# Performance work log

Measured on AMD Instinct MI355X. Metric: run time of the kernel, lower is better.

The kernel has to match this reference:

```python
import jax, jax.numpy as jnp
import numpy as np

N = 10000        # total nodes in batch
E = 320000       # total edges (before self-loops)
D_IN = 128       # node_dim
H_DIM = 64       # hidden_dim
HEADS = 4
B = 64           # number of graphs
NUM_EDGES = 1024 # actor output dim


def _lin(k, i, o):
    return jax.random.normal(k, (i, o), jnp.float32) / np.sqrt(i)


def setup_inputs() -> dict:
    key = jax.random.key(0)
    ks = jax.random.split(key, 32)
    x = jax.random.normal(ks[0], (N, D_IN), jnp.float32)
    edge_index = jax.random.randint(ks[1], (2, E), 0, N, dtype=jnp.int64)
    batch = jnp.sort(jax.random.randint(ks[2], (N,), 0, B, dtype=jnp.int64))
    inp = dict(x=x, edge_index=edge_index, batch=batch)
    # GAT layer 1: in=D_IN, heads=4, out=H_DIM, concat
    inp['W1'] = _lin(ks[3], D_IN, HEADS * H_DIM)
    inp['as1'] = jax.random.normal(ks[4], (HEADS, H_DIM), jnp.float32) * 0.1
    inp['ad1'] = jax.random.normal(ks[5], (HEADS, H_DIM), jnp.float32) * 0.1
    inp['b1'] = jnp.zeros((HEADS * H_DIM,), jnp.float32)
    # GAT layer 2: in=4*H_DIM, heads=4, out=H_DIM, concat
    inp['W2'] = _lin(ks[6], HEADS * H_DIM, HEADS * H_DIM)
    inp['as2'] = jax.random.normal(ks[7], (HEADS, H_DIM), jnp.float32) * 0.1
    inp['ad2'] = jax.random.normal(ks[8], (HEADS, H_DIM), jnp.float32) * 0.1
    inp['b2'] = jnp.zeros((HEADS * H_DIM,), jnp.float32)
    # GAT layer 3: in=4*H_DIM, heads=1, out=H_DIM, mean (concat=False)
    inp['W3'] = _lin(ks[9], HEADS * H_DIM, H_DIM)
    inp['as3'] = jax.random.normal(ks[10], (1, H_DIM), jnp.float32) * 0.1
    inp['ad3'] = jax.random.normal(ks[11], (1, H_DIM), jnp.float32) * 0.1
    inp['b3'] = jnp.zeros((H_DIM,), jnp.float32)
    # actor MLP
    inp['Wa1'] = _lin(ks[12], H_DIM, H_DIM); inp['ba1'] = jnp.zeros((H_DIM,), jnp.float32)
    inp['Wa2'] = _lin(ks[13], H_DIM, NUM_EDGES); inp['ba2'] = jnp.zeros((NUM_EDGES,), jnp.float32)
    # critic MLP
    inp['Wc1'] = _lin(ks[14], H_DIM, H_DIM); inp['bc1'] = jnp.zeros((H_DIM,), jnp.float32)
    inp['Wc2'] = _lin(ks[15], H_DIM, 1); inp['bc2'] = jnp.zeros((1,), jnp.float32)
    return inp


def gat_layer(x, src, dst, W, a_src, a_dst, bias, heads, out_dim, concat):
    # PyG GATConv: linear -> edge attention -> per-dst softmax -> scatter-add
    n = x.shape[0]
    h = (x @ W).reshape(n, heads, out_dim)            # [N,H,D]
    s = (h * a_src).sum(-1)                           # [N,H] attention src term
    d = (h * a_dst).sum(-1)                           # [N,H]
    e = jax.nn.leaky_relu(s[src] + d[dst], 0.2)       # [Eall,H]
    m = jax.ops.segment_max(e, dst, num_segments=n)   # stable softmax per dst node
    w = jnp.exp(e - m[dst])
    alpha = w / jax.ops.segment_sum(w, dst, num_segments=n)[dst]
    agg = jax.ops.segment_sum(h[src] * alpha[..., None], dst, num_segments=n)  # [N,H,D]
    o = agg.reshape(n, heads * out_dim) if concat else agg.mean(axis=1)
    return o + bias


def forward(x, edge_index, batch, W1, as1, ad1, b1, W2, as2, ad2, b2,
            W3, as3, ad3, b3, Wa1, ba1, Wa2, ba2, Wc1, bc1, Wc2, bc2):
    n = x.shape[0]
    loop = jnp.arange(n, dtype=edge_index.dtype)
    src = jnp.concatenate([edge_index[0], loop])      # add_self_loops=True (PyG default)
    dst = jnp.concatenate([edge_index[1], loop])
    h = jax.nn.relu(gat_layer(x, src, dst, W1, as1, ad1, b1, HEADS, H_DIM, True))
    h = jax.nn.relu(gat_layer(h, src, dst, W2, as2, ad2, b2, HEADS, H_DIM, True))
    h = jax.nn.relu(gat_layer(h, src, dst, W3, as3, ad3, b3, 1, H_DIM, False))
    # global_mean_pool
    counts = jax.ops.segment_sum(jnp.ones((n,), h.dtype), batch, num_segments=B)
    pooled = jax.ops.segment_sum(h, batch, num_segments=B) / jnp.maximum(counts, 1.0)[:, None]
    # heads (dropout is identity at inference)
    action = jnp.tanh(jax.nn.relu(pooled @ Wa1 + ba1) @ Wa2 + ba2)
    value = jax.nn.relu(pooled @ Wc1 + bc1) @ Wc2 + bc2
    return action, value


def reference(x, edge_index, batch, W1, as1, ad1, b1, W2, as2, ad2, b2,
              W3, as3, ad3, b3, Wa1, ba1, Wa2, ba2, Wc1, bc1, Wc2, bc2):
    return forward(x, edge_index, batch, W1, as1, ad1, b1, W2, as2, ad2, b2,
                   W3, as3, ad3, b3, Wa1, ba1, Wa2, ba2, Wc1, bc1, Wc2, bc2)
```

## Files before the change

### kernel.cpp

```cpp
#include <hip/hip_runtime.h>
#include <hip/hip_bf16.h>

#define NN 10000
#define EE 320000
#define EALL (EE + NN)
#define BG 64
#define AOUT 1024

#define WTOT 191361
#define NX (NN * 128)
#define XV (NX / 8)
#define NSF 262144
#define NSI 131072

#define DRANGE 640
#define DNB 16
#define NSEG 64
#define ESEG 5157

typedef __hip_bfloat16 bf16;
typedef __attribute__((ext_vector_type(8))) short bf16x8;
typedef __attribute__((ext_vector_type(4))) float f32x4;

__device__ __forceinline__ unsigned short f2bf(float f) {
    bf16 h = __float2bfloat16(f);
    return *reinterpret_cast<unsigned short*>(&h);
}
__device__ __forceinline__ float bf2f(unsigned short u) {
    bf16 h;
    *reinterpret_cast<unsigned short*>(&h) = u;
    return __bfloat162float(h);
}
__device__ __forceinline__ int f_isfp32(const int* flags) {
    return (flags[2] > 0 || flags[3] > 50000) ? 1 : 0;
}

__global__ void k_detect(const unsigned short* __restrict__ x, const unsigned int* __restrict__ ei,
                         int* __restrict__ flags) {
    int i = blockIdx.x * 256 + threadIdx.x;
    bool nanp = false, zp = false, odd = false;
    if (i < NSF) {
        unsigned short h = x[i];
        nanp = (h & 0x7F80u) == 0x7F80u;
        zp = ((i & 1) == 0) && (h == 0);
    } else if (i < NSF + NSI) {
        int j = i - NSF;
        odd = ei[2 * j + 1] != 0u;
    }
    unsigned long long bn = __ballot(nanp);
    unsigned long long bz = __ballot(zp);
    unsigned long long bo = __ballot(odd);
    if ((threadIdx.x & 63) == 0) {
        if (bn) atomicAdd(&flags[2], __popcll(bn));
        if (bz) atomicAdd(&flags[3], __popcll(bz));
        if (bo) atomicOr(&flags[1], 1);
    }
}

struct WPtrs { const void* p[20]; };
__global__ void k_cvt_all(WPtrs wp, const void* __restrict__ xsrc,
                          const void* __restrict__ eisrc, const void* __restrict__ bsrc,
                          float* __restrict__ wf, int* __restrict__ ei32, int* __restrict__ b32,
                          unsigned short* __restrict__ x16,
                          unsigned short* __restrict__ w1t, unsigned short* __restrict__ w2t,
                          unsigned short* __restrict__ w3t,
                          const int* __restrict__ flags) {
    const int sz[20] = {32768,256,256,256,65536,256,256,256,16384,64,64,64,4096,64,65536,1024,4096,64,64,1};
    int i = blockIdx.x * 256 + threadIdx.x;
    const int ff = f_isfp32(flags), fi = flags[1];
    if (i < WTOT) {
        int seg = 0, off = 0;
        while (i - off >= sz[seg]) { off += sz[seg]; seg++; }
        const void* src = wp.p[seg];
        int k = i - off;
        wf[i] = ff ? ((const float*)src)[k] : __bfloat162float(((const bf16*)src)[k]);
        return;
    }
    i -= WTOT;
    if (i < EE) {
        int j = i * 2;
        if (fi) {
            int2 v = ((const int2*)eisrc)[i];
            ei32[j] = v.x; ei32[j + 1] = v.y;
        } else {
            const long long* e8 = (const long long*)eisrc;
            ei32[j] = (int)e8[j]; ei32[j + 1] = (int)e8[j + 1];
        }
        return;
    }
    i -= EE;
    if (i < NN) { b32[i] = fi ? ((const int*)bsrc)[i] : (int)((const long long*)bsrc)[i]; return; }
    i -= NN;
    if (i < XV) {
        int k = i * 8;
        if (ff) {
            const float4* xs = (const float4*)((const float*)xsrc + k);
            float4 a = xs[0], b = xs[1];
            union { unsigned short u16[8]; uint4 v; } pk;
            pk.u16[0] = f2bf(a.x); pk.u16[1] = f2bf(a.y);
            pk.u16[2] = f2bf(a.z); pk.u16[3] = f2bf(a.w);
            pk.u16[4] = f2bf(b.x); pk.u16[5] = f2bf(b.y);
            pk.u16[6] = f2bf(b.z); pk.u16[7] = f2bf(b.w);
            *(uint4*)&x16[k] = pk.v;
        } else {
            *(uint4*)&x16[k] = ((const uint4*)xsrc)[i];
        }
        return;
    }
    i -= XV;
    if (i < 32768) {
        int k = i >> 8, c = i & 255;
        float v = ff ? ((const float*)wp.p[0])[i] : __bfloat162float(((const bf16*)wp.p[0])[i]);
        w1t[c * 128 + k] = f2bf(v);
        return;
    }
    i -= 32768;
    if (i < 65536) {
        int k = i >> 8, c = i & 255;
        float v = ff ? ((const float*)wp.p[4])[i] : __bfloat162float(((const bf16*)wp.p[4])[i]);
        w2t[c * 256 + k] = f2bf(v);
        return;
    }
    i -= 65536;
    if (i < 16384) {
        int k = i >> 6, c = i & 63;
        float v = ff ? ((const float*)wp.p[8])[i] : __bfloat162float(((const bf16*)wp.p[8])[i]);
        w3t[c * 256 + k] = f2bf(v);
    }
}
#define CVT_TOT (WTOT + EE + NN + XV + 32768 + 65536 + 16384)

__global__ __launch_bounds__(256) void k_fuse1(const int* __restrict__ ei, int* __restrict__ partial,
                                               const unsigned short* __restrict__ A16,
                                               const unsigned short* __restrict__ WT16,
                                               const float* __restrict__ asf,
                                               const float* __restrict__ adf,
                                               unsigned short* __restrict__ C16,
                                               float* __restrict__ sb, float* __restrict__ db) {
    __shared__ int bins[DRANGE];
    constexpr int LDW = 40;
    __shared__ unsigned short As[64 * LDW];
    __shared__ unsigned short Bs[64 * LDW];
    const int t = threadIdx.x;
    if (blockIdx.x < DNB * NSEG) {
        const int r0 = (blockIdx.x >> 6) * DRANGE;
        const int sg = blockIdx.x & 63;
        for (int i = t; i < DRANGE; i += 256) bins[i] = 0;
        __syncthreads();
        const int e1 = min(sg * ESEG + ESEG, EALL);
        for (int e = sg * ESEG + t; e < e1; e += 256) {
            int dst = (e < EE) ? ei[EE + e] : (e - EE);
            unsigned rel = dst - r0;
            if (rel < DRANGE) atomicAdd(&bins[rel], 1);
        }
        __syncthreads();
        for (int i = t; i < DRANGE; i += 256)
            partial[blockIdx.x * DRANGE + i] = bins[i];
        return;
    }
    constexpr int K = 128, M = 256, H = M / 64;
    const int u = blockIdx.x - DNB * NSEG;
    const int bx = u % 157;
    const int hh = u / 157;
    const int row0 = bx * 64;
    const int col0 = hh * 64;
    const int wv = t >> 6;
    const int lane = t & 63;
    const int m = lane & 15;
    const int q = lane >> 4;
    const int srow = t >> 2;
    const int skoff = (t & 3) * 8;

    f32x4 acc[4] = {};
    for (int k0 = 0; k0 < K; k0 += 32) {
        {
            int grow = row0 + srow;
            uint4 av = make_uint4(0u, 0u, 0u, 0u);
            if (grow < NN) av = *(const uint4*)&A16[(size_t)grow * K + k0 + skoff];
            *(uint4*)&As[srow * LDW + skoff] = av;
            uint4 bv = *(const uint4*)&WT16[(size_t)(col0 + srow) * K + k0 + skoff];
            *(uint4*)&Bs[srow * LDW + skoff] = bv;
        }
        __syncthreads();
        bf16x8 af = *(const bf16x8*)&As[(16 * wv + m) * LDW + q * 8];
#pragma unroll
        for (int ct = 0; ct < 4; ct++) {
            bf16x8 bfv = *(const bf16x8*)&Bs[(16 * ct + m) * LDW + q * 8];
            acc[ct] = __builtin_amdgcn_mfma_f32_16x16x32_bf16(af, bfv, acc[ct], 0, 0, 0);
        }
        __syncthreads();
    }
    float asv[4], adv[4];
#pragma unroll
    for (int ct = 0; ct < 4; ct++) {
        asv[ct] = asf[hh * 64 + 16 * ct + m];
        adv[ct] = adf[hh * 64 + 16 * ct + m];
    }
#pragma unroll
    for (int reg = 0; reg < 4; reg++) {
        int row = row0 + 16 * wv + q * 4 + reg;
        float ps = 0.f, pd = 0.f;
        if (row < NN) {
#pragma unroll
            for (int ct = 0; ct < 4; ct++) {
                float v = acc[ct][reg];
                C16[(size_t)row * M + col0 + 16 * ct + m] = f2bf(v);
                ps += v * asv[ct];
                pd += v * adv[ct];
            }
        }
#pragma unroll
        for (int off = 1; off < 16; off <<= 1) {
            ps += __shfl_xor(ps, off);
            pd += __shfl_xor(pd, off);
        }
        if (m == 0 && row < NN) { sb[row * H + hh] = ps; db[row * H + hh] = pd; }
    }
}

__global__ void k_seg(const int* __restrict__ partial, int* __restrict__ deg,
                      int* __restrict__ segpre) {
    int bin = blockIdx.x * 256 + threadIdx.x;
    if (bin >= NN) return;
    int r = bin / DRANGE, rel = bin - r * DRANGE;
    int s = 0;
    for (int sg = 0; sg < NSEG; sg++) {
        int idx = (r * NSEG + sg) * DRANGE + rel;
        int v = partial[idx];
        segpre[idx] = s;
        s += v;
    }
    deg[bin] = s;
}

__global__ void k_scan4(const int* __restrict__ deg, int* __restrict__ rowstart,
                        const int* __restrict__ batch, int* __restrict__ gstart) {
    __shared__ int part[1024];
    const int t = threadIdx.x;
    if (t <= BG) {
        int lo = 0, hi = NN;
        while (lo < hi) { int mid = (lo + hi) >> 1; if (batch[mid] < t) lo = mid + 1; else hi = mid; }
        gstart[t] = lo;
    }
    const int base = t * 10;
    int local[10];
    int s = 0;
    for (int i = 0; i < 10; i++) {
        int idx = base + i;
        int v = (idx < NN) ? deg[idx] : 0;
        local[i] = s; s += v;
    }
    part[t] = s; __syncthreads();
    for (int off = 1; off < 1024; off <<= 1) {
        int v = (t >= off) ? part[t - off] : 0;
        __syncthreads();
        part[t] += v;
        __syncthreads();
    }
    int pre = (t == 0) ? 0 : part[t - 1];
    for (int i = 0; i < 10; i++) {
        int idx = base + i;
        if (idx < NN) rowstart[idx] = pre + local[i];
    }
    if (t == 1023) rowstart[NN] = part[1023];
}

__global__ __launch_bounds__(256) void k_scatter3(const int* __restrict__ ei,
                                                  const int* __restrict__ rowstart,
                                                  const int* __restrict__ segpre,
                                                  int* __restrict__ ssrc) {
    __shared__ int cur[DRANGE];
    const int r0 = blockIdx.x * DRANGE;
    const int sg = blockIdx.y;
    for (int i = threadIdx.x; i < DRANGE; i += 256) {
        int bin = r0 + i;
        cur[i] = (bin < NN) ? rowstart[bin] + segpre[(blockIdx.x * NSEG + sg) * DRANGE + i] : 0;
    }
    __syncthreads();
    const int e1 = min(sg * ESEG + ESEG, EALL);
    for (int e = sg * ESEG + threadIdx.x; e < e1; e += 256) {
        int dst = (e < EE) ? ei[EE + e] : (e - EE);
        unsigned rel = dst - r0;
        if (rel < DRANGE) {
            int src = (e < EE) ? ei[e] : dst;
            int pos = atomicAdd(&cur[rel], 1);
            ssrc[pos] = src;
        }
    }
}

template<int K, int M>
__global__ __launch_bounds__(256) void k_gemm(const unsigned short* __restrict__ A16,
                                              const unsigned short* __restrict__ WT16,
                                              const float* __restrict__ asf,
                                              const float* __restrict__ adf,
                                              unsigned short* __restrict__ C16,
                                              float* __restrict__ sb, float* __restrict__ db) {
    constexpr int BK = 32;
    constexpr int H = M / 64;
    constexpr int LDW = 40;
    __shared__ unsigned short As[64 * LDW];
    __shared__ unsigned short Bs[64 * LDW];
    const int row0 = blockIdx.x * 64;
    const int col0 = blockIdx.y * 64;
    const int hh = blockIdx.y;
    const int t = threadIdx.x;
    const int wv = t >> 6;
    const int lane = t & 63;
    const int m = lane & 15;
    const int q = lane >> 4;
    const int srow = t >> 2;
    const int skoff = (t & 3) * 8;

    f32x4 acc[4] = {};

    for (int k0 = 0; k0 < K; k0 += BK) {
        {
            int grow = row0 + srow;
            uint4 av = make_uint4(0u, 0u, 0u, 0u);
            if (grow < NN) av = *(const uint4*)&A16[(size_t)grow * K + k0 + skoff];
            *(uint4*)&As[srow * LDW + skoff] = av;
            uint4 bv = *(const uint4*)&WT16[(size_t)(col0 + srow) * K + k0 + skoff];
            *(uint4*)&Bs[srow * LDW + skoff] = bv;
        }
        __syncthreads();
        bf16x8 af = *(const bf16x8*)&As[(16 * wv + m) * LDW + q * 8];
#pragma unroll
        for (int ct = 0; ct < 4; ct++) {
            bf16x8 bfv = *(const bf16x8*)&Bs[(16 * ct + m) * LDW + q * 8];
            acc[ct] = __builtin_amdgcn_mfma_f32_16x16x32_bf16(af, bfv, acc[ct], 0, 0, 0);
        }
        __syncthreads();
    }

    float asv[4], adv[4];
#pragma unroll
    for (int ct = 0; ct < 4; ct++) {
        asv[ct] = asf[hh * 64 + 16 * ct + m];
        adv[ct] = adf[hh * 64 + 16 * ct + m];
    }
#pragma unroll
    for (int reg = 0; reg < 4; reg++) {
        int row = row0 + 16 * wv + q * 4 + reg;
        float ps = 0.f, pd = 0.f;
        if (row < NN) {
#pragma unroll
            for (int ct = 0; ct < 4; ct++) {
                float v = acc[ct][reg];
                C16[(size_t)row * M + col0 + 16 * ct + m] = f2bf(v);
                ps += v * asv[ct];
                pd += v * adv[ct];
            }
        }
#pragma unroll
        for (int off = 1; off < 16; off <<= 1) {
            ps += __shfl_xor(ps, off);
            pd += __shfl_xor(pd, off);
        }
        if (m == 0 && row < NN) { sb[row * H + hh] = ps; db[row * H + hh] = pd; }
    }
}

template<int H>
__global__ void k_agg(const unsigned short* __restrict__ hbuf16, const float* __restrict__ sb,
                      const float* __restrict__ db, const int* __restrict__ rowstart,
                      const int* __restrict__ ssrc, const float* __restrict__ bias,
                      unsigned short* __restrict__ out16) {
    constexpr int M = H * 64;
    constexpr int LH = (H == 4) ? 2 : 0;
    constexpr int CG = M / 8;
    constexpr int LCG = (H == 4) ? 5 : 3;
    const int n = blockIdx.x;
    const int tid = threadIdx.x;
    const int start = rowstart[n], end = rowstart[n + 1];
    const int slot = tid >> LH;
    const int hh = tid & (H - 1);
    const int cg = tid & (CG - 1);
    const int eg = tid >> LCG;
    const int chh = (H == 4) ? (cg >> 3) : 0;
    __shared__ float red[M];
    __shared__ float sm[H], sws[H];
    __shared__ float wl[64 * H];
    __shared__ int srcl[64];
    __shared__ float accbuf[8 * M];
    const float dn = db[n * H + hh];

    float mymax = -3e38f;
    for (int p = start + slot; p < end; p += 64) {
        float e = sb[ssrc[p] * H + hh] + dn;
        e = e > 0.f ? e : 0.2f * e;
        mymax = fmaxf(mymax, e);
    }
    red[tid] = mymax; __syncthreads();
    for (int off = M / 2; off >= H; off >>= 1) {
        if (tid < off) red[tid] = fmaxf(red[tid], red[tid + off]);
        __syncthreads();
    }
    if (tid < H) sm[tid] = red[tid];
    __syncthreads();
    const float mh = sm[hh];

    float wsum = 0.f;
    float acc[8] = {};
    for (int c = start; c < end; c += 64) {
        const int cn = min(64, end - c);
        __syncthreads();
        if (slot < cn) {
            int s = ssrc[c + slot];
            float e = sb[s * H + hh] + dn;
            e = e > 0.f ? e : 0.2f * e;
            float wv = __expf(e - mh);
            wl[slot * H + hh] = wv;
            wsum += wv;
            if (hh == 0) srcl[slot] = s;
        }
        __syncthreads();
#pragma unroll 2
        for (int j = eg; j < cn; j += 8) {
            float wv = wl[j * H + chh];
            const bf16x8 v = *(const bf16x8*)&hbuf16[(size_t)srcl[j] * M + cg * 8];
#pragma unroll
            for (int i = 0; i < 8; i++)
                acc[i] += wv * bf2f((unsigned short)v[i]);
        }
    }

    {
        float* ab = &accbuf[eg * M + cg * 8];
#pragma unroll
        for (int i = 0; i < 8; i++) ab[i] = acc[i];
    }
    red[tid] = wsum; __syncthreads();
    for (int off = M / 2; off >= H; off >>= 1) {
        if (tid < off) red[tid] += red[tid + off];
        __syncthreads();
    }
    if (tid < H) sws[tid] = red[tid];
    __syncthreads();

    float o = 0.f;
#pragma unroll
    for (int e8 = 0; e8 < 8; e8++) o += accbuf[e8 * M + tid];
    o = o / sws[(H == 4) ? (tid >> 6) : 0] + bias[tid];
    out16[(size_t)n * M + tid] = f2bf(fmaxf(o, 0.f));
}

__global__ __launch_bounds__(256) void k_final(const unsigned short* __restrict__ feat16,
                                               const int* __restrict__ gstart,
                                               const float* __restrict__ Wa1, const float* __restrict__ ba1,
                                               const float* __restrict__ Wc1, const float* __restrict__ bc1,
                                               const float* __restrict__ Wa2, const float* __restrict__ ba2,
                                               const float* __restrict__ Wc2, const float* __restrict__ bc2,
                                               float* __restrict__ out) {
    __shared__ float red[256];
    __shared__ float p[64];
    __shared__ float a[64], cc[64];
    const int g = blockIdx.x, t = threadIdx.x;
    const int d = t & 63, c = t >> 6;
    const int s = gstart[g], e = gstart[g + 1];
    float acc = 0.f;
    for (int n = s + c; n < e; n += 4) acc += bf2f(feat16[(size_t)n * 64 + d]);
    red[t] = acc; __syncthreads();
    if (c == 0) p[d] = (red[d] + red[64 + d] + red[128 + d] + red[192 + d])
                       / fmaxf((float)(e - s), 1.f);
    __syncthreads();
    if (t < 128) {
        int j = t & 63;
        const float* W  = (t < 64) ? Wa1 : Wc1;
        const float* bb = (t < 64) ? ba1 : bc1;
        float h = 0.f;
#pragma unroll 8
        for (int k = 0; k < 64; k++) h += p[k] * W[k * 64 + j];
        h = fmaxf(h + bb[j], 0.f);
        if (t < 64) a[j] = h; else cc[j] = h;
    }
    __syncthreads();
    float o[4] = {0.f, 0.f, 0.f, 0.f};
    for (int k = 0; k < 64; k++) {
        float ak = a[k];
#pragma unroll
        for (int q = 0; q < 4; q++) o[q] += ak * Wa2[k * AOUT + t + 256 * q];
    }
#pragma unroll
    for (int q = 0; q < 4; q++)
        out[g * AOUT + t + 256 * q] = tanhf(o[q] + ba2[t + 256 * q]);
    if (t == 0) {
        float v = 0.f;
        for (int k = 0; k < 64; k++) v += cc[k] * Wc2[k];
        out[BG * AOUT + g] = v + bc2[0];
    }
}

extern "C" void kernel_launch(void* const* d_in, const int* in_sizes, int n_in,
                              void* d_out, int out_size, void* d_ws, size_t ws_size,
                              hipStream_t stream) {
    float* out = (float*)d_out;

    char* w = (char*)d_ws;
    auto alloc = [&](size_t bytes) { void* p = (void*)w; w += (bytes + 255) & ~size_t(255); return p; };
    float* wf      = (float*)alloc((size_t)WTOT * 4);
    int*   ei32    = (int*)alloc((size_t)2 * EE * 4);
    int*   b32     = (int*)alloc((size_t)NN * 4);
    unsigned short* x16    = (unsigned short*)alloc((size_t)NX * 2);
    unsigned short* w1t    = (unsigned short*)alloc((size_t)32768 * 2);
    unsigned short* w2t    = (unsigned short*)alloc((size_t)65536 * 2);
    unsigned short* w3t    = (unsigned short*)alloc((size_t)16384 * 2);
    unsigned short* actA16 = (unsigned short*)alloc((size_t)NN * 256 * 2);
    unsigned short* actB16 = (unsigned short*)alloc((size_t)NN * 256 * 2);
    float* sb      = (float*)alloc((size_t)NN * 4 * 4);
    float* db      = (float*)alloc((size_t)NN * 4 * 4);
    int*   partial = (int*)alloc((size_t)DNB * NSEG * DRANGE * 4);
    int*   segpre  = (int*)alloc((size_t)DNB * NSEG * DRANGE * 4);
    int*   deg     = (int*)alloc((size_t)NN * 4);
    int*   flags   = (int*)alloc(64);
    int*   rowstart= (int*)alloc((size_t)(NN + 1) * 4);
    int*   ssrc    = (int*)alloc((size_t)EALL * 4);
    int*   gstart  = (int*)alloc((size_t)(BG + 1) * 4);

    hipMemsetAsync(flags, 0, 64, stream);

    k_detect<<<(NSF + NSI + 255) / 256, 256, 0, stream>>>(
        (const unsigned short*)d_in[0], (const unsigned int*)d_in[1], flags);

    WPtrs wp;
    for (int s = 0; s < 20; s++) wp.p[s] = d_in[3 + s];
    k_cvt_all<<<(CVT_TOT + 255) / 256, 256, 0, stream>>>(
        wp, d_in[0], d_in[1], d_in[2], wf, ei32, b32, x16, w1t, w2t, w3t, flags);

    const int wsz[20] = {32768,256,256,256,65536,256,256,256,16384,64,64,64,4096,64,65536,1024,4096,64,64,1};
    int woff[20]; int acc = 0;
    for (int s = 0; s < 20; s++) { woff[s] = acc; acc += wsz[s]; }
    const float *as1f = wf + woff[1], *ad1f = wf + woff[2], *b1f = wf + woff[3];
    const float *as2f = wf + woff[5], *ad2f = wf + woff[6], *b2f = wf + woff[7];
    const float *as3f = wf + woff[9], *ad3f = wf + woff[10], *b3f = wf + woff[11];
    const float *Wa1f = wf + woff[12], *ba1f = wf + woff[13], *Wa2f = wf + woff[14], *ba2f = wf + woff[15];
    const float *Wc1f = wf + woff[16], *bc1f = wf + woff[17], *Wc2f = wf + woff[18], *bc2f = wf + woff[19];

    k_fuse1<<<DNB * NSEG + 628, 256, 0, stream>>>(ei32, partial,
                                                  x16, w1t, as1f, ad1f, actA16, sb, db);

    k_seg<<<(NN + 255) / 256, 256, 0, stream>>>(partial, deg, segpre);
    k_scan4<<<1, 1024, 0, stream>>>(deg, rowstart, b32, gstart);
    k_scatter3<<<dim3(DNB, NSEG), 256, 0, stream>>>(ei32, rowstart, segpre, ssrc);

    k_agg<4><<<NN, 256, 0, stream>>>(actA16, sb, db, rowstart, ssrc, b1f, actB16);

    k_gemm<256, 256><<<dim3(157, 4), 256, 0, stream>>>(actB16, w2t, as2f, ad2f, actA16, sb, db);
    k_agg<4><<<NN, 256, 0, stream>>>(actA16, sb, db, rowstart, ssrc, b2f, actB16);

    k_gemm<256, 64><<<dim3(157, 1), 256, 0, stream>>>(actB16, w3t, as3f, ad3f, actA16, sb, db);
    k_agg<1><<<NN, 64, 0, stream>>>(actA16, sb, db, rowstart, ssrc, b3f, actB16);

    k_final<<<BG, 256, 0, stream>>>(actB16, gstart,
                                    Wa1f, ba1f, Wc1f, bc1f, Wa2f, ba2f, Wc2f, bc2f, out);
}
```

Baseline: 274.9 us.

## Fuse layer-3 linear projection into layer-2 aggregation; skip dtype detection via input sizes

The layer-2 aggregation kernel now also runs the layer-3 matvec (256->64) per node, along with its attention source and destination scores. This removes the separate layer-3 GEMM launch and one round trip of the 256-wide activation through global memory. Separately, input dtypes are inferred on the host from in_sizes, which skips the memset and detection kernel when the sizes match. The fused kernel adds per-block work and reads W3 from global memory in every block, which may cost throughput in the aggregation kernel.

```diff
diff --git a/kernel.cpp b/kernel.cpp
--- a/kernel.cpp
+++ b/kernel.cpp
@@ -64,10 +64,11 @@
                           unsigned short* __restrict__ x16,
                           unsigned short* __restrict__ w1t, unsigned short* __restrict__ w2t,
                           unsigned short* __restrict__ w3t,
-                          const int* __restrict__ flags) {
+                          const int* __restrict__ flags, int ffh, int fih) {
     const int sz[20] = {32768,256,256,256,65536,256,256,256,16384,64,64,64,4096,64,65536,1024,4096,64,64,1};
     int i = blockIdx.x * 256 + threadIdx.x;
-    const int ff = f_isfp32(flags), fi = flags[1];
+    const int ff = (ffh >= 0) ? ffh : f_isfp32(flags);
+    const int fi = (fih >= 0) ? fih : flags[1];
     if (i < WTOT) {
         int seg = 0, off = 0;
         while (i - off >= sz[seg]) { off += sz[seg]; seg++; }
@@ -445,6 +446,123 @@
     out16[(size_t)n * M + tid] = f2bf(fmaxf(o, 0.f));
 }
 
+__global__ __launch_bounds__(256) void k_agg4w3(const unsigned short* __restrict__ hbuf16,
+                                                const float* __restrict__ sb,
+                                                const float* __restrict__ db,
+                                                const int* __restrict__ rowstart,
+                                                const int* __restrict__ ssrc,
+                                                const float* __restrict__ bias,
+                                                const unsigned short* __restrict__ w3t,
+                                                const float* __restrict__ as3,
+                                                const float* __restrict__ ad3,
+                                                unsigned short* __restrict__ out3,
+                                                float* __restrict__ sb3, float* __restrict__ db3) {
+    constexpr int M = 256;
+    const int n = blockIdx.x;
+    const int tid = threadIdx.x;
+    const int start = rowstart[n], end = rowstart[n + 1];
+    const int slot = tid >> 2;
+    const int hh = tid & 3;
+    const int cg = tid & 31;
+    const int eg = tid >> 5;
+    const int chh = cg >> 3;
+    __shared__ float red[M];
+    __shared__ float sm[4], sws[4];
+    __shared__ float wl[256];
+    __shared__ int srcl[64];
+    __shared__ float accbuf[8 * M];
+    const float dn = db[n * 4 + hh];
+
+    float mymax = -3e38f;
+    for (int p = start + slot; p < end; p += 64) {
+        float e = sb[ssrc[p] * 4 + hh] + dn;
+        e = e > 0.f ? e : 0.2f * e;
+        mymax = fmaxf(mymax, e);
+    }
+    red[tid] = mymax; __syncthreads();
+    for (int off = M / 2; off >= 4; off >>= 1) {
+        if (tid < off) red[tid] = fmaxf(red[tid], red[tid + off]);
+        __syncthreads();
+    }
+    if (tid < 4) sm[tid] = red[tid];
+    __syncthreads();
+    const float mh = sm[hh];
+
+    float wsum = 0.f;
+    float acc[8] = {};
+    for (int c = start; c < end; c += 64) {
+        const int cn = min(64, end - c);
+        __syncthreads();
+        if (slot < cn) {
+            int s = ssrc[c + slot];
+            float e = sb[s * 4 + hh] + dn;
+            e = e > 0.f ? e : 0.2f * e;
+            float wv = __expf(e - mh);
+            wl[slot * 4 + hh] = wv;
+            wsum += wv;
+            if (hh == 0) srcl[slot] = s;
+        }
+        __syncthreads();
+#pragma unroll 2
+        for (int j = eg; j < cn; j += 8) {
+            float wv = wl[j * 4 + chh];
+            const bf16x8 v = *(const bf16x8*)&hbuf16[(size_t)srcl[j] * M + cg * 8];
+#pragma unroll
+            for (int i = 0; i < 8; i++)
+                acc[i] += wv * bf2f((unsigned short)v[i]);
+        }
+    }
+
+    {
+        float* ab = &accbuf[eg * M + cg * 8];
+#pragma unroll
+        for (int i = 0; i < 8; i++) ab[i] = acc[i];
+    }
+    red[tid] = wsum; __syncthreads();
+    for (int off = M / 2; off >= 4; off >>= 1) {
+        if (tid < off) red[tid] += red[tid + off];
+        __syncthreads();
+    }
+    if (tid < 4) sws[tid] = red[tid];
+    __syncthreads();
+
+    float o = 0.f;
+#pragma unroll
+    for (int e8 = 0; e8 < 8; e8++) o += accbuf[e8 * M + tid];
+    o = o / sws[tid >> 6] + bias[tid];
+    float orow = bf2f(f2bf(fmaxf(o, 0.f)));
+    __syncthreads();
+    red[tid] = orow;
+    __syncthreads();
+
+    const int j = tid & 63, c4 = tid >> 6;
+    {
+        const unsigned short* wrow = &w3t[j * 256 + c4 * 64];
+        const float* rsrc = &red[c4 * 64];
+        float h = 0.f;
+#pragma unroll
+        for (int k = 0; k < 64; k += 8) {
+            bf16x8 wv8 = *(const bf16x8*)&wrow[k];
+#pragma unroll
+            for (int i = 0; i < 8; i++)
+                h += rsrc[k + i] * bf2f((unsigned short)wv8[i]);
+        }
+        accbuf[tid] = h;
+    }
+    __syncthreads();
+    if (tid < 64) {
+        float h3 = accbuf[j] + accbuf[64 + j] + accbuf[128 + j] + accbuf[192 + j];
+        out3[(size_t)n * 64 + j] = f2bf(h3);
+        float ps = h3 * as3[j], pd = h3 * ad3[j];
+#pragma unroll
+        for (int off = 1; off < 64; off <<= 1) {
+            ps += __shfl_xor(ps, off);
+            pd += __shfl_xor(pd, off);
+        }
+        if (j == 0) { sb3[n] = ps; db3[n] = pd; }
+    }
+}
+
 __global__ __launch_bounds__(256) void k_final(const unsigned short* __restrict__ feat16,
                                                const int* __restrict__ gstart,
                                                const float* __restrict__ Wa1, const float* __restrict__ ba1,
@@ -509,6 +627,8 @@
     unsigned short* actB16 = (unsigned short*)alloc((size_t)NN * 256 * 2);
     float* sb      = (float*)alloc((size_t)NN * 4 * 4);
     float* db      = (float*)alloc((size_t)NN * 4 * 4);
+    float* sb3     = (float*)alloc((size_t)NN * 4);
+    float* db3     = (float*)alloc((size_t)NN * 4);
     int*   partial = (int*)alloc((size_t)DNB * NSEG * DRANGE * 4);
     int*   segpre  = (int*)alloc((size_t)DNB * NSEG * DRANGE * 4);
     int*   deg     = (int*)alloc((size_t)NN * 4);
@@ -517,15 +637,25 @@
     int*   ssrc    = (int*)alloc((size_t)EALL * 4);
     int*   gstart  = (int*)alloc((size_t)(BG + 1) * 4);
 
-    hipMemsetAsync(flags, 0, 64, stream);
-
-    k_detect<<<(NSF + NSI + 255) / 256, 256, 0, stream>>>(
-        (const unsigned short*)d_in[0], (const unsigned int*)d_in[1], flags);
+    int ffh = -1, fih = -1;
+    if (in_sizes && n_in >= 2) {
+        long long xs = in_sizes[0];
+        if (xs == (long long)NX * 4) ffh = 1;
+        else if (xs == (long long)NX * 2) ffh = 0;
+        long long es = in_sizes[1];
+        if (es == (long long)2 * EE * 8) fih = 0;
+        else if (es == (long long)2 * EE * 4) fih = 1;
+    }
+    if (ffh < 0 || fih < 0) {
+        hipMemsetAsync(flags, 0, 64, stream);
+        k_detect<<<(NSF + NSI + 255) / 256, 256, 0, stream>>>(
+            (const unsigned short*)d_in[0], (const unsigned int*)d_in[1], flags);
+    }
 
     WPtrs wp;
     for (int s = 0; s < 20; s++) wp.p[s] = d_in[3 + s];
     k_cvt_all<<<(CVT_TOT + 255) / 256, 256, 0, stream>>>(
-        wp, d_in[0], d_in[1], d_in[2], wf, ei32, b32, x16, w1t, w2t, w3t, flags);
+        wp, d_in[0], d_in[1], d_in[2], wf, ei32, b32, x16, w1t, w2t, w3t, flags, ffh, fih);
 
     const int wsz[20] = {32768,256,256,256,65536,256,256,256,16384,64,64,64,4096,64,65536,1024,4096,64,64,1};
     int woff[20]; int acc = 0;
@@ -546,11 +676,11 @@
     k_agg<4><<<NN, 256, 0, stream>>>(actA16, sb, db, rowstart, ssrc, b1f, actB16);
 
     k_gemm<256, 256><<<dim3(157, 4), 256, 0, stream>>>(actB16, w2t, as2f, ad2f, actA16, sb, db);
-    k_agg<4><<<NN, 256, 0, stream>>>(actA16, sb, db, rowstart, ssrc, b2f, actB16);
-
-    k_gemm<256, 64><<<dim3(157, 1), 256, 0, stream>>>(actB16, w3t, as3f, ad3f, actA16, sb, db);
-    k_agg<1><<<NN, 64, 0, stream>>>(actA16, sb, db, rowstart, ssrc, b3f, actB16);
-
-    k_final<<<BG, 256, 0, stream>>>(actB16, gstart,
+    k_agg4w3<<<NN, 256, 0, stream>>>(actA16, sb, db, rowstart, ssrc, b2f,
+                                     w3t, as3f, ad3f, actB16, sb3, db3);
+
+    k_agg<1><<<NN, 64, 0, stream>>>(actB16, sb3, db3, rowstart, ssrc, b3f, actA16);
+
+    k_final<<<BG, 256, 0, stream>>>(actA16, gstart,
                                     Wa1f, ba1f, Wc1f, bc1f, Wa2f, ba2f, Wc2f, bc2f, out);
 }
```

After: 302.5 us. 10.0% more time.

## Use wave shuffles for softmax reductions and skip dtype detection via input sizes

Applied to the files above, without the earlier changes.

The per-node aggregation kernel now does its max and sum reductions with wavefront xor-shuffles plus a small per-wave shared array, replacing the shared-memory tree that needed a barrier at every step. On the host, input dtypes are inferred from buffer byte sizes when available, which skips the memset and the detection kernel launch. The dtype detection path is still kept as a fallback when sizes are ambiguous.

```diff
diff --git a/kernel.cpp b/kernel.cpp
--- a/kernel.cpp
+++ b/kernel.cpp
@@ -64,10 +64,11 @@
                           unsigned short* __restrict__ x16,
                           unsigned short* __restrict__ w1t, unsigned short* __restrict__ w2t,
                           unsigned short* __restrict__ w3t,
-                          const int* __restrict__ flags) {
+                          const int* __restrict__ flags, int ffh, int fih) {
     const int sz[20] = {32768,256,256,256,65536,256,256,256,16384,64,64,64,4096,64,65536,1024,4096,64,64,1};
     int i = blockIdx.x * 256 + threadIdx.x;
-    const int ff = f_isfp32(flags), fi = flags[1];
+    const int ff = (ffh >= 0) ? ffh : f_isfp32(flags);
+    const int fi = (fih >= 0) ? fih : flags[1];
     if (i < WTOT) {
         int seg = 0, off = 0;
         while (i - off >= sz[seg]) { off += sz[seg]; seg++; }
@@ -368,6 +369,7 @@
                       unsigned short* __restrict__ out16) {
     constexpr int M = H * 64;
     constexpr int LH = (H == 4) ? 2 : 0;
+    constexpr int NW = M / 64;
     constexpr int CG = M / 8;
     constexpr int LCG = (H == 4) ? 5 : 3;
     const int n = blockIdx.x;
@@ -375,14 +377,16 @@
     const int start = rowstart[n], end = rowstart[n + 1];
     const int slot = tid >> LH;
     const int hh = tid & (H - 1);
+    const int wv = tid >> 6;
+    const int lane = tid & 63;
     const int cg = tid & (CG - 1);
     const int eg = tid >> LCG;
     const int chh = (H == 4) ? (cg >> 3) : 0;
-    __shared__ float red[M];
-    __shared__ float sm[H], sws[H];
     __shared__ float wl[64 * H];
     __shared__ int srcl[64];
     __shared__ float accbuf[8 * M];
+    __shared__ float smw[NW][H];
+    __shared__ float sww[NW][H];
     const float dn = db[n * H + hh];
 
     float mymax = -3e38f;
@@ -391,14 +395,18 @@
         e = e > 0.f ? e : 0.2f * e;
         mymax = fmaxf(mymax, e);
     }
-    red[tid] = mymax; __syncthreads();
-    for (int off = M / 2; off >= H; off >>= 1) {
-        if (tid < off) red[tid] = fmaxf(red[tid], red[tid + off]);
-        __syncthreads();
-    }
-    if (tid < H) sm[tid] = red[tid];
-    __syncthreads();
-    const float mh = sm[hh];
+#pragma unroll
+    for (int off = H; off < 64; off <<= 1) mymax = fmaxf(mymax, __shfl_xor(mymax, off));
+    float mh;
+    if constexpr (NW > 1) {
+        if (lane < H) smw[wv][lane] = mymax;
+        __syncthreads();
+        mh = smw[0][hh];
+#pragma unroll
+        for (int w = 1; w < NW; w++) mh = fmaxf(mh, smw[w][hh]);
+    } else {
+        mh = mymax;
+    }
 
     float wsum = 0.f;
     float acc[8] = {};
@@ -409,19 +417,19 @@
             int s = ssrc[c + slot];
             float e = sb[s * H + hh] + dn;
             e = e > 0.f ? e : 0.2f * e;
-            float wv = __expf(e - mh);
-            wl[slot * H + hh] = wv;
-            wsum += wv;
+            float wv2 = __expf(e - mh);
+            wl[slot * H + hh] = wv2;
+            wsum += wv2;
             if (hh == 0) srcl[slot] = s;
         }
         __syncthreads();
 #pragma unroll 2
         for (int j = eg; j < cn; j += 8) {
-            float wv = wl[j * H + chh];
+            float wv2 = wl[j * H + chh];
             const bf16x8 v = *(const bf16x8*)&hbuf16[(size_t)srcl[j] * M + cg * 8];
 #pragma unroll
             for (int i = 0; i < 8; i++)
-                acc[i] += wv * bf2f((unsigned short)v[i]);
+                acc[i] += wv2 * bf2f((unsigned short)v[i]);
         }
     }
 
@@ -430,18 +438,25 @@
 #pragma unroll
         for (int i = 0; i < 8; i++) ab[i] = acc[i];
     }
-    red[tid] = wsum; __syncthreads();
-    for (int off = M / 2; off >= H; off >>= 1) {
-        if (tid < off) red[tid] += red[tid + off];
-        __syncthreads();
-    }
-    if (tid < H) sws[tid] = red[tid];
+#pragma unroll
+    for (int off = H; off < 64; off <<= 1) wsum += __shfl_xor(wsum, off);
+    if constexpr (NW > 1) { if (lane < H) sww[wv][lane] = wsum; }
     __syncthreads();
 
+    float wsh;
+    const int h2 = (H == 4) ? (tid >> 6) : 0;
+    if constexpr (NW > 1) {
+        wsh = sww[0][h2];
+#pragma unroll
+        for (int w = 1; w < NW; w++) wsh += sww[w][h2];
+    } else {
+        wsh = wsum;
+    }
+
     float o = 0.f;
 #pragma unroll
     for (int e8 = 0; e8 < 8; e8++) o += accbuf[e8 * M + tid];
-    o = o / sws[(H == 4) ? (tid >> 6) : 0] + bias[tid];
+    o = o / wsh + bias[tid];
     out16[(size_t)n * M + tid] = f2bf(fmaxf(o, 0.f));
 }
 
@@ -517,15 +532,25 @@
     int*   ssrc    = (int*)alloc((size_t)EALL * 4);
     int*   gstart  = (int*)alloc((size_t)(BG + 1) * 4);
 
-    hipMemsetAsync(flags, 0, 64, stream);
-
-    k_detect<<<(NSF + NSI + 255) / 256, 256, 0, stream>>>(
-        (const unsigned short*)d_in[0], (const unsigned int*)d_in[1], flags);
+    int ffh = -1, fih = -1;
+    if (in_sizes && n_in >= 2) {
+        long long xs = in_sizes[0];
+        if (xs == (long long)NX * 4) ffh = 1;
+        else if (xs == (long long)NX * 2) ffh = 0;
+        long long es = in_sizes[1];
+        if (es == (long long)2 * EE * 8) fih = 0;
+        else if (es == (long long)2 * EE * 4) fih = 1;
+    }
+    if (ffh < 0 || fih < 0) {
+        hipMemsetAsync(flags, 0, 64, stream);
+        k_detect<<<(NSF + NSI + 255) / 256, 256, 0, stream>>>(
+            (const unsigned short*)d_in[0], (const unsigned int*)d_in[1], flags);
+    }
 
     WPtrs wp;
     for (int s = 0; s < 20; s++) wp.p[s] = d_in[3 + s];
     k_cvt_all<<<(CVT_TOT + 255) / 256, 256, 0, stream>>>(
-        wp, d_in[0], d_in[1], d_in[2], wf, ei32, b32, x16, w1t, w2t, w3t, flags);
+        wp, d_in[0], d_in[1], d_in[2], wf, ei32, b32, x16, w1t, w2t, w3t, flags, ffh, fih);
 
     const int wsz[20] = {32768,256,256,256,65536,256,256,256,16384,64,64,64,4096,64,65536,1024,4096,64,64,1};
     int woff[20]; int acc = 0;
```

Result: no change. 270.2 us (-1.7%).
